# Kernel tuning notes

Measured on AMD Instinct MI355X. Metric: run time of the kernel, lower is better.

Reference implementation:

```python
import jax, jax.numpy as jnp
import numpy as np

NUM_HEAD = 8

def _ln(h, g, b):
    m = jnp.mean(h, axis=-1, keepdims=True)
    v = jnp.mean(jnp.square(h - m), axis=-1, keepdims=True)
    return (h - m) * jax.lax.rsqrt(v + 1e-5) * g + b

def _lin(h, W, b):
    return h @ W.T + b

def _styl(h, e, se_w, se_b, sn_g, sn_b, so_w, so_b):
    # StylizationBlock (AdaLN-zero): emb -> SiLU -> Linear -> scale/shift
    eo = _lin(jax.nn.silu(e), se_w, se_b)[:, None, :]  # [B,1,2D]
    scale, shift = jnp.split(eo, 2, axis=-1)
    h = _ln(h, sn_g, sn_b) * (1.0 + scale) + shift
    return _lin(jax.nn.silu(h), so_w, so_b)

def setup_inputs():
    key = jax.random.key(0)
    ks = iter(jax.random.split(key, 48))
    T, B, N, D = 256, 64, 77, 512
    FF_SA, FF = 1024, 2048
    w = lambda *s: jax.random.normal(next(ks), s, dtype=jnp.float32) * 0.02
    z = lambda *s: jnp.zeros(s, jnp.float32)
    o = lambda *s: jnp.ones(s, jnp.float32)
    return dict(
        x=jax.random.normal(next(ks), (T, B, D), dtype=jnp.float32),
        xf=jax.random.normal(next(ks), (N, B, D), dtype=jnp.float32),
        emb=jax.random.normal(next(ks), (1, B, D), dtype=jnp.float32),
        sa_in_w=w(3 * D, D), sa_in_b=z(3 * D), sa_out_w=w(D, D), sa_out_b=z(D),
        sa_l1_w=w(FF_SA, D), sa_l1_b=z(FF_SA), sa_l2_w=w(D, FF_SA), sa_l2_b=z(D),
        sa_n1_g=o(D), sa_n1_b=z(D), sa_n2_g=o(D), sa_n2_b=z(D),
        ca_norm_g=o(D), ca_norm_b=z(D), ca_tnorm_g=o(D), ca_tnorm_b=z(D),
        ca_q_w=w(D, D), ca_q_b=z(D), ca_k_w=w(D, D), ca_k_b=z(D), ca_v_w=w(D, D), ca_v_b=z(D),
        ca_se_w=w(2 * D, D), ca_se_b=z(2 * D), ca_sn_g=o(D), ca_sn_b=z(D), ca_so_w=w(D, D), ca_so_b=z(D),
        ff_l1_w=w(FF, D), ff_l1_b=z(FF), ff_l2_w=w(D, FF), ff_l2_b=z(D),
        ff_se_w=w(2 * D, D), ff_se_b=z(2 * D), ff_sn_g=o(D), ff_sn_b=z(D), ff_so_w=w(D, D), ff_so_b=z(D),
    )

def reference(x, xf, emb, sa_in_w, sa_in_b, sa_out_w, sa_out_b, sa_l1_w, sa_l1_b, sa_l2_w, sa_l2_b, sa_n1_g, sa_n1_b, sa_n2_g, sa_n2_b, ca_norm_g, ca_norm_b, ca_tnorm_g, ca_tnorm_b, ca_q_w, ca_q_b, ca_k_w, ca_k_b, ca_v_w, ca_v_b, ca_se_w, ca_se_b, ca_sn_g, ca_sn_b, ca_so_w, ca_so_b, ff_l1_w, ff_l1_b, ff_l2_w, ff_l2_b, ff_se_w, ff_se_b, ff_sn_g, ff_sn_b, ff_so_w, ff_so_b):
    T = x.shape[0]
    # --- MLD self-attention path: concat motion tokens, text tokens, time emb ---
    src = jnp.concatenate([x, xf, emb], axis=0)  # [S,B,D], S = T+N+1
    S, B, D = src.shape
    dh = D // NUM_HEAD
    qkv = _lin(src, sa_in_w, sa_in_b)
    q, k, v = jnp.split(qkv, 3, axis=-1)
    q = q.reshape(S, B, NUM_HEAD, dh) * (dh ** -0.5)
    k = k.reshape(S, B, NUM_HEAD, dh)
    v = v.reshape(S, B, NUM_HEAD, dh)
    att = jax.nn.softmax(jnp.einsum('sbhd,tbhd->bhst', q, k), axis=-1)
    o = jnp.einsum('bhst,tbhd->sbhd', att, v).reshape(S, B, D)
    src = _ln(src + _lin(o, sa_out_w, sa_out_b), sa_n1_g, sa_n1_b)
    ffh = _lin(jax.nn.relu(_lin(src, sa_l1_w, sa_l1_b)), sa_l2_w, sa_l2_b)
    src = _ln(src + ffh, sa_n2_g, sa_n2_b)
    xb = src[:T].transpose(1, 0, 2)   # [B,T,D]
    xfb = xf.transpose(1, 0, 2)       # [B,N,D]
    eb = emb[0]                       # [B,D]
    # --- Linear temporal cross-attention ---
    xn = _ln(xb, ca_norm_g, ca_norm_b)
    tn = _ln(xfb, ca_tnorm_g, ca_tnorm_b)
    qc = jax.nn.softmax(_lin(xn, ca_q_w, ca_q_b).reshape(B, T, NUM_HEAD, dh), axis=-1)
    kc = jax.nn.softmax(_lin(tn, ca_k_w, ca_k_b).reshape(B, -1, NUM_HEAD, dh), axis=1)
    vc = _lin(tn, ca_v_w, ca_v_b).reshape(B, -1, NUM_HEAD, dh)
    ctx = jnp.einsum('bnhd,bnhl->bhdl', kc, vc)
    y = jnp.einsum('bthd,bhdl->bthl', qc, ctx).reshape(B, T, D)
    xb = xb + _styl(y, eb, ca_se_w, ca_se_b, ca_sn_g, ca_sn_b, ca_so_w, ca_so_b)
    # --- FFN with stylization ---
    y = _lin(jax.nn.gelu(_lin(xb, ff_l1_w, ff_l1_b), approximate=False), ff_l2_w, ff_l2_b)
    xb = xb + _styl(y, eb, ff_se_w, ff_se_b, ff_sn_g, ff_sn_b, ff_so_w, ff_so_b)
    return xb.transpose(1, 0, 2)  # [T,B,D]
```

## Files before the change

### kernel.cpp

```cpp
#include <hip/hip_runtime.h>
#include <hip/hip_bf16.h>
#include <cstddef>

#define TT 256
#define BB 64
#define NN 77
#define DD 512
#define SS 334
#define HH 8
#define M1 (SS*BB)
#define M2 (BB*TT)
#define FF 2048

#define REG 10944512ULL

typedef __attribute__((ext_vector_type(4))) float f32x4;
typedef __attribute__((ext_vector_type(8))) short bf16x8;
typedef __attribute__((ext_vector_type(8))) unsigned short u16x8;

__device__ inline unsigned short f2bf(float f) {
  __hip_bfloat16 h = __float2bfloat16(f);
  return *reinterpret_cast<unsigned short*>(&h);
}
__device__ inline float bf2f(unsigned short u) {
  return __uint_as_float(((unsigned)u) << 16);
}

__global__ __launch_bounds__(256) void cvt4_kernel(
    const float* s0, unsigned short* d0, int n0,
    const float* s1, unsigned short* d1, int n1,
    const float* s2, unsigned short* d2, int n2,
    const float* s3, unsigned short* d3, int n3) {
  const float* s; unsigned short* d; int n;
  switch (blockIdx.y) {
    case 0: s = s0; d = d0; n = n0; break;
    case 1: s = s1; d = d1; n = n1; break;
    case 2: s = s2; d = d2; n = n2; break;
    default: s = s3; d = d3; n = n3; break;
  }
  for (int i = (blockIdx.x * 256 + threadIdx.x) * 4; i < n; i += gridDim.x * 1024) {
    float4 v = *(const float4*)(s + i);
    ushort4 u;
    u.x = f2bf(v.x); u.y = f2bf(v.y); u.z = f2bf(v.z); u.w = f2bf(v.w);
    *(ushort4*)(d + i) = u;
  }
}

__global__ __launch_bounds__(256) void concat_src_kernel(
    const float* __restrict__ x, const float* __restrict__ xf,
    const float* __restrict__ emb, float* __restrict__ src,
    unsigned short* __restrict__ srcbf) {
  int idx = blockIdx.x * 256 + threadIdx.x;
  if (idx >= SS * BB * 128) return;
  int c4 = idx & 127;
  int row = idx >> 7;
  int s = row >> 6, b = row & 63;
  const float* p;
  if (s < TT)            p = x   + ((size_t)(s * BB + b)) * DD;
  else if (s < TT + NN)  p = xf  + ((size_t)((s - TT) * BB + b)) * DD;
  else                   p = emb + (size_t)b * DD;
  float4 v = ((const float4*)p)[c4];
  ((float4*)(src + (size_t)row * DD))[c4] = v;
  ushort4 u;
  u.x = f2bf(v.x); u.y = f2bf(v.y); u.z = f2bf(v.z); u.w = f2bf(v.w);
  ((ushort4*)(srcbf + (size_t)row * DD))[c4] = u;
}

template<int EPI, bool CBF>
__global__ __launch_bounds__(256) void gemm_bf(
    const unsigned short* __restrict__ A, const unsigned short* __restrict__ W,
    const float* __restrict__ bias, void* __restrict__ Cp_, void* __restrict__ C2,
    int M, int K, int ldc) {
  __shared__ unsigned short As[8][128][8];
  __shared__ unsigned short Bs[8][128][8];
  const int tid = threadIdx.x;
  int bxt, byt;
  {
    int total = gridDim.x * gridDim.y;
    int raw = blockIdx.y * gridDim.x + blockIdx.x;
    if ((total & 7) == 0) {
      int lid = (raw & 7) * (total >> 3) + (raw >> 3);
      bxt = lid % gridDim.x;
      byt = lid / gridDim.x;
    } else { bxt = blockIdx.x; byt = blockIdx.y; }
  }
  const int bm = byt * 128;
  const int bn = bxt * 128;
  const int lane = tid & 63;
  const int wave = tid >> 6;
  const int wr = wave >> 1, wc = wave & 1;
  const int q = lane >> 4, lr = lane & 15;

  f32x4 acc[4][4];
#pragma unroll
  for (int m = 0; m < 4; ++m)
#pragma unroll
    for (int n = 0; n < 4; ++n) acc[m][n] = (f32x4){0.f, 0.f, 0.f, 0.f};

  const int srow = tid >> 1;
  const int sk = (tid & 1) * 32;
  const int c0 = (tid & 1) * 4;
  int arow = bm + srow; if (arow >= M) arow = M - 1;
  const unsigned short* Ag = A + (size_t)arow * K + sk;
  const unsigned short* Wg = W + (size_t)(bn + srow) * K + sk;

  for (int k0 = 0; k0 < K; k0 += 64) {
    u16x8 a0 = *(const u16x8*)(Ag + k0);
    u16x8 a1 = *(const u16x8*)(Ag + k0 + 8);
    u16x8 a2 = *(const u16x8*)(Ag + k0 + 16);
    u16x8 a3 = *(const u16x8*)(Ag + k0 + 24);
    u16x8 b0 = *(const u16x8*)(Wg + k0);
    u16x8 b1 = *(const u16x8*)(Wg + k0 + 8);
    u16x8 b2 = *(const u16x8*)(Wg + k0 + 16);
    u16x8 b3 = *(const u16x8*)(Wg + k0 + 24);
    __syncthreads();
    *(u16x8*)&As[c0 + 0][srow][0] = a0;
    *(u16x8*)&As[c0 + 1][srow][0] = a1;
    *(u16x8*)&As[c0 + 2][srow][0] = a2;
    *(u16x8*)&As[c0 + 3][srow][0] = a3;
    *(u16x8*)&Bs[c0 + 0][srow][0] = b0;
    *(u16x8*)&Bs[c0 + 1][srow][0] = b1;
    *(u16x8*)&Bs[c0 + 2][srow][0] = b2;
    *(u16x8*)&Bs[c0 + 3][srow][0] = b3;
    __syncthreads();
#pragma unroll
    for (int ks = 0; ks < 2; ++ks) {
      bf16x8 af[4], bf[4];
#pragma unroll
      for (int m = 0; m < 4; ++m)
        af[m] = *(const bf16x8*)&As[ks * 4 + q][wr * 64 + m * 16 + lr][0];
#pragma unroll
      for (int n = 0; n < 4; ++n)
        bf[n] = *(const bf16x8*)&Bs[ks * 4 + q][wc * 64 + n * 16 + lr][0];
#pragma unroll
      for (int m = 0; m < 4; ++m)
#pragma unroll
        for (int n = 0; n < 4; ++n)
          acc[m][n] = __builtin_amdgcn_mfma_f32_16x16x32_bf16(af[m], bf[n], acc[m][n], 0, 0, 0);
    }
  }

  if (EPI == 6) {
    const int hcol = (bn >> 6) + wc;
#pragma unroll
    for (int m = 0; m < 4; ++m) {
#pragma unroll
      for (int i = 0; i < 4; ++i) {
        float vv[4];
        float mx = -1e30f;
#pragma unroll
        for (int n = 0; n < 4; ++n) {
          float v = acc[m][n][i] + bias[bn + wc * 64 + n * 16 + lr];
          vv[n] = v; mx = fmaxf(mx, v);
        }
#pragma unroll
        for (int off = 8; off; off >>= 1) mx = fmaxf(mx, __shfl_xor(mx, off));
        float sum = 0.f;
#pragma unroll
        for (int n = 0; n < 4; ++n) { vv[n] = __expf(vv[n] - mx); sum += vv[n]; }
#pragma unroll
        for (int off = 8; off; off >>= 1) sum += __shfl_xor(sum, off);
        float inv = 1.f / sum;
        const int row = bm + wr * 64 + m * 16 + q * 4 + i;
        const int t = row & 255, b2 = row >> 8;
        unsigned short* dst =
            (unsigned short*)Cp_ + (((size_t)(b2 * 8 + hcol) * 256 + t) << 6);
#pragma unroll
        for (int n = 0; n < 4; ++n)
          dst[n * 16 + lr] = f2bf(vv[n] * inv);
      }
    }
    return;
  }

#pragma unroll
  for (int m = 0; m < 4; ++m) {
#pragma unroll
    for (int n = 0; n < 4; ++n) {
      const int col = bn + wc * 64 + n * 16 + lr;
      const float bb = bias[col];
#pragma unroll
      for (int i = 0; i < 4; ++i) {
        const int row = bm + wr * 64 + m * 16 + q * 4 + i;
        if (row < M) {
          float v = acc[m][n][i] + bb;
          if (EPI == 1) v = fmaxf(v, 0.f);
          if (EPI == 2) v = 0.5f * v * (1.f + erff(v * 0.70710678118f));
          if (EPI == 7) v *= 0.125f;
          if (EPI <= 2 || EPI == 7) {
            if (CBF) ((unsigned short*)Cp_)[(size_t)row * ldc + col] = f2bf(v);
            else     ((float*)Cp_)[(size_t)row * ldc + col] = v;
          } else if (EPI == 3) {
            ((float*)Cp_)[(size_t)row * ldc + col] += v;
          } else if (EPI == 4) {
            float* C = (float*)Cp_ + (size_t)row * ldc + col;
            float o = *C + v; *C = o;
            ((unsigned short*)C2)[(size_t)row * ldc + col] = f2bf(o);
          } else {
            float o = ((const float*)Cp_)[(size_t)row * ldc + col] + v;
            int t = row & 255, b2 = row >> 8;
            ((float*)C2)[((size_t)(t * BB + b2)) * DD + col] = o;
          }
        }
      }
    }
  }
}

__global__ __launch_bounds__(256) void attn_mfma_kernel(
    const unsigned short* __restrict__ Qb, const unsigned short* __restrict__ KVb,
    unsigned short* __restrict__ Ob) {
  __shared__ unsigned short Qs[256][72];
  __shared__ unsigned short Ks[64][72];
  __shared__ unsigned short Vt[64][72];
  __shared__ unsigned short Ps[4][16][72];
  const int bh = blockIdx.x, b = bh >> 3, h = bh & 7;
  const int tid = threadIdx.x;
  const int wave = tid >> 6, lane = tid & 63;
  const int q = lane >> 4, lr = lane & 15;
  const int sr = tid >> 2;
  const int c0 = (tid & 3) << 4;
#pragma unroll
  for (int it = 0; it < 8; ++it) {
    int v = it * 256 + tid;
    int row = v >> 3, col = (v & 7) * 8;
    u16x8 d8 = *(const u16x8*)(Qb + ((size_t)(row * BB + b)) * 512 + h * 64 + col);
    *(u16x8*)&Qs[row][col] = d8;
  }
  f32x4 oacc[4][4];
#pragma unroll
  for (int m = 0; m < 4; ++m)
#pragma unroll
    for (int dt = 0; dt < 4; ++dt) oacc[m][dt] = (f32x4){0.f, 0.f, 0.f, 0.f};
  float m_r[4][4], l_r[4][4];
#pragma unroll
  for (int m = 0; m < 4; ++m)
#pragma unroll
    for (int i = 0; i < 4; ++i) { m_r[m][i] = -1e30f; l_r[m][i] = 0.f; }

  for (int kt = 0; kt < 6; ++kt) {
    __syncthreads();
    {
      int t = kt * 64 + sr;
      u16x8 k0 = {0, 0, 0, 0, 0, 0, 0, 0}, k1 = k0, w0 = k0, w1 = k0;
      if (t < SS) {
        const unsigned short* kp = KVb + ((size_t)(t * BB + b)) * 1024 + h * 64 + c0;
        k0 = *(const u16x8*)kp; k1 = *(const u16x8*)(kp + 8);
        w0 = *(const u16x8*)(kp + 512); w1 = *(const u16x8*)(kp + 520);
      }
      *(u16x8*)&Ks[sr][c0] = k0;
      *(u16x8*)&Ks[sr][c0 + 8] = k1;
#pragma unroll
      for (int j = 0; j < 8; ++j) Vt[c0 + j][sr] = w0[j];
#pragma unroll
      for (int j = 0; j < 8; ++j) Vt[c0 + 8 + j][sr] = w1[j];
    }
    __syncthreads();
#pragma unroll
    for (int m = 0; m < 4; ++m) {
      f32x4 sacc[4];
#pragma unroll
      for (int ct = 0; ct < 4; ++ct) sacc[ct] = (f32x4){0.f, 0.f, 0.f, 0.f};
#pragma unroll
      for (int kc = 0; kc < 2; ++kc) {
        bf16x8 aq = *(const bf16x8*)&Qs[wave * 64 + m * 16 + lr][kc * 32 + q * 8];
#pragma unroll
        for (int ct = 0; ct < 4; ++ct) {
          bf16x8 bk = *(const bf16x8*)&Ks[ct * 16 + lr][kc * 32 + q * 8];
          sacc[ct] = __builtin_amdgcn_mfma_f32_16x16x32_bf16(aq, bk, sacc[ct], 0, 0, 0);
        }
      }
      if (kt == 5) {
#pragma unroll
        for (int ct = 0; ct < 4; ++ct)
          if (320 + ct * 16 + lr >= SS) {
#pragma unroll
            for (int i = 0; i < 4; ++i) sacc[ct][i] = -1e30f;
          }
      }
      float pexp[4][4];
#pragma unroll
      for (int i = 0; i < 4; ++i) {
        float mt = fmaxf(fmaxf(sacc[0][i], sacc[1][i]), fmaxf(sacc[2][i], sacc[3][i]));
#pragma unroll
        for (int off = 8; off; off >>= 1) mt = fmaxf(mt, __shfl_xor(mt, off));
        float mn = fmaxf(m_r[m][i], mt);
        float rescale = __expf(m_r[m][i] - mn);
        m_r[m][i] = mn;
        float se = 0.f;
#pragma unroll
        for (int ct = 0; ct < 4; ++ct) {
          float e = __expf(sacc[ct][i] - mn);
          pexp[ct][i] = e;
          se += e;
        }
#pragma unroll
        for (int off = 8; off; off >>= 1) se += __shfl_xor(se, off);
        l_r[m][i] = l_r[m][i] * rescale + se;
#pragma unroll
        for (int dt = 0; dt < 4; ++dt) oacc[m][dt][i] *= rescale;
      }
#pragma unroll
      for (int ct = 0; ct < 4; ++ct)
#pragma unroll
        for (int i = 0; i < 4; ++i)
          Ps[wave][q * 4 + i][ct * 16 + lr] = f2bf(pexp[ct][i]);
#pragma unroll
      for (int kc = 0; kc < 2; ++kc) {
        bf16x8 ap = *(const bf16x8*)&Ps[wave][lr][kc * 32 + q * 8];
#pragma unroll
        for (int dt = 0; dt < 4; ++dt) {
          bf16x8 bv = *(const bf16x8*)&Vt[dt * 16 + lr][kc * 32 + q * 8];
          oacc[m][dt] = __builtin_amdgcn_mfma_f32_16x16x32_bf16(ap, bv, oacc[m][dt], 0, 0, 0);
        }
      }
    }
  }
#pragma unroll
  for (int m = 0; m < 4; ++m) {
#pragma unroll
    for (int i = 0; i < 4; ++i) {
      int s = wave * 64 + m * 16 + q * 4 + i;
      float inv = 1.f / l_r[m][i];
      unsigned short* op = Ob + ((size_t)(s * BB + b)) * 512 + h * 64;
#pragma unroll
      for (int dt = 0; dt < 4; ++dt)
        op[dt * 16 + lr] = f2bf(oacc[m][dt][i] * inv);
    }
  }
}

__global__ __launch_bounds__(256) void lin_y_mfma(
    const unsigned short* __restrict__ qch, const unsigned short* __restrict__ ctxT,
    float* __restrict__ y) {
  __shared__ unsigned short Qs[256][72];
  __shared__ unsigned short Cs[64][72];
  const int bh = blockIdx.x, b = bh >> 3, h = bh & 7;
  const int tid = threadIdx.x;
  const int wave = tid >> 6, lane = tid & 63;
  const int q = lane >> 4, lr = lane & 15;
  {
    const unsigned short* qp = qch + (size_t)bh * 16384;
#pragma unroll
    for (int it = 0; it < 8; ++it) {
      int v = it * 256 + tid;
      u16x8 d8 = *(const u16x8*)(qp + v * 8);
      *(u16x8*)&Qs[v >> 3][(v & 7) * 8] = d8;
    }
    const unsigned short* cp = ctxT + (size_t)bh * 4096;
#pragma unroll
    for (int it = 0; it < 2; ++it) {
      int v = it * 256 + tid;
      u16x8 d8 = *(const u16x8*)(cp + v * 8);
      *(u16x8*)&Cs[v >> 3][(v & 7) * 8] = d8;
    }
  }
  __syncthreads();
  f32x4 acc[4][4];
#pragma unroll
  for (int m = 0; m < 4; ++m)
#pragma unroll
    for (int n = 0; n < 4; ++n) acc[m][n] = (f32x4){0.f, 0.f, 0.f, 0.f};
#pragma unroll
  for (int kc = 0; kc < 2; ++kc) {
    bf16x8 af[4], bf[4];
#pragma unroll
    for (int m = 0; m < 4; ++m)
      af[m] = *(const bf16x8*)&Qs[wave * 64 + m * 16 + lr][kc * 32 + q * 8];
#pragma unroll
    for (int n = 0; n < 4; ++n)
      bf[n] = *(const bf16x8*)&Cs[n * 16 + lr][kc * 32 + q * 8];
#pragma unroll
    for (int m = 0; m < 4; ++m)
#pragma unroll
      for (int n = 0; n < 4; ++n)
        acc[m][n] = __builtin_amdgcn_mfma_f32_16x16x32_bf16(af[m], bf[n], acc[m][n], 0, 0, 0);
  }
#pragma unroll
  for (int m = 0; m < 4; ++m) {
#pragma unroll
    for (int n = 0; n < 4; ++n) {
#pragma unroll
      for (int i = 0; i < 4; ++i) {
        int t = wave * 64 + m * 16 + q * 4 + i;
        y[((size_t)(b * TT + t)) * DD + h * 64 + n * 16 + lr] = acc[m][n][i];
      }
    }
  }
}

__global__ __launch_bounds__(256) void gemm_se_kernel(
    const float* __restrict__ emb,
    const float* __restrict__ w0, const float* __restrict__ b0, float* __restrict__ c0_,
    const float* __restrict__ w1, const float* __restrict__ b1, float* __restrict__ c1_) {
  __shared__ float As[16][64];
  __shared__ float Ws[16][64];
  const float* W    = blockIdx.y ? w1 : w0;
  const float* bias = blockIdx.y ? b1 : b0;
  float* C          = blockIdx.y ? c1_ : c0_;
  const int tid = threadIdx.x;
  const int bn = blockIdx.x << 6;
  const int lr = tid >> 2;
  const int lk = (tid & 3) << 2;
  const float* Ap = emb + (size_t)lr * 512 + lk;
  const float* Wp = W + (size_t)(bn + lr) * 512 + lk;
  const int tx = tid & 15, ty = tid >> 4;
  float c[4][4] = {};
  for (int k0 = 0; k0 < 512; k0 += 16) {
    float4 av = *(const float4*)(Ap + k0);
    av.x = av.x / (1.f + __expf(-av.x));
    av.y = av.y / (1.f + __expf(-av.y));
    av.z = av.z / (1.f + __expf(-av.z));
    av.w = av.w / (1.f + __expf(-av.w));
    float4 wv = *(const float4*)(Wp + k0);
    __syncthreads();
    As[lk + 0][lr] = av.x; As[lk + 1][lr] = av.y;
    As[lk + 2][lr] = av.z; As[lk + 3][lr] = av.w;
    Ws[lk + 0][lr] = wv.x; Ws[lk + 1][lr] = wv.y;
    Ws[lk + 2][lr] = wv.z; Ws[lk + 3][lr] = wv.w;
    __syncthreads();
#pragma unroll
    for (int k = 0; k < 16; ++k) {
      const float4 a = *(const float4*)&As[k][ty << 2];
      const float4 w = *(const float4*)&Ws[k][tx << 2];
      c[0][0] += a.x * w.x; c[0][1] += a.x * w.y; c[0][2] += a.x * w.z; c[0][3] += a.x * w.w;
      c[1][0] += a.y * w.x; c[1][1] += a.y * w.y; c[1][2] += a.y * w.z; c[1][3] += a.y * w.w;
      c[2][0] += a.z * w.x; c[2][1] += a.z * w.y; c[2][2] += a.z * w.z; c[2][3] += a.z * w.w;
      c[3][0] += a.w * w.x; c[3][1] += a.w * w.y; c[3][2] += a.w * w.z; c[3][3] += a.w * w.w;
    }
  }
#pragma unroll
  for (int i = 0; i < 4; ++i) {
    int row = (ty << 2) + i;
    float* Cp = C + (size_t)row * 1024 + bn + (tx << 2);
#pragma unroll
    for (int j = 0; j < 4; ++j)
      Cp[j] = c[i][j] + bias[bn + (tx << 2) + j];
  }
}

__global__ __launch_bounds__(64) void ln_kernel(
    const float* __restrict__ in, const float* __restrict__ res,
    float* __restrict__ out, const float* __restrict__ g,
    const float* __restrict__ beta, unsigned short* __restrict__ obf) {
  const int row = blockIdx.x;
  const int lane = threadIdx.x;
  const float* ip = in + (size_t)row * DD;
  float v[8];
  float s = 0.f, ss = 0.f;
#pragma unroll
  for (int u = 0; u < 2; ++u) {
    int d = u * 256 + lane * 4;
    float4 a = *(const float4*)(ip + d);
    if (res) {
      float4 r = *(const float4*)(res + (size_t)row * DD + d);
      a.x += r.x; a.y += r.y; a.z += r.z; a.w += r.w;
    }
    v[u * 4 + 0] = a.x; v[u * 4 + 1] = a.y; v[u * 4 + 2] = a.z; v[u * 4 + 3] = a.w;
    s += a.x + a.y + a.z + a.w;
    ss += a.x * a.x + a.y * a.y + a.z * a.z + a.w * a.w;
  }
#pragma unroll
  for (int off = 32; off; off >>= 1) { s += __shfl_xor(s, off); ss += __shfl_xor(ss, off); }
  float mean = s * (1.f / 512.f);
  float var = ss * (1.f / 512.f) - mean * mean;
  float rstd = rsqrtf(var + 1e-5f);
  float* op = out + (size_t)row * DD;
#pragma unroll
  for (int u = 0; u < 2; ++u) {
    int d = u * 256 + lane * 4;
    float4 o4;
    o4.x = (v[u * 4 + 0] - mean) * rstd * g[d + 0] + beta[d + 0];
    o4.y = (v[u * 4 + 1] - mean) * rstd * g[d + 1] + beta[d + 1];
    o4.z = (v[u * 4 + 2] - mean) * rstd * g[d + 2] + beta[d + 2];
    o4.w = (v[u * 4 + 3] - mean) * rstd * g[d + 3] + beta[d + 3];
    *(float4*)(op + d) = o4;
    if (obf) {
      ushort4 u4;
      u4.x = f2bf(o4.x); u4.y = f2bf(o4.y); u4.z = f2bf(o4.z); u4.w = f2bf(o4.w);
      *(ushort4*)(obf + (size_t)row * DD + d) = u4;
    }
  }
}

template<bool WF32>
__global__ __launch_bounds__(64) void t2bln_kernel(
    const float* __restrict__ in, float* __restrict__ raw,
    unsigned short* __restrict__ obf, const float* __restrict__ g,
    const float* __restrict__ beta, int Rr) {
  const int rp = blockIdx.x;
  const int b = rp / Rr, r = rp % Rr;
  const float* ip = in + ((size_t)(r * BB + b)) * DD;
  const int lane = threadIdx.x;
  float v[8];
  float s = 0.f, ss = 0.f;
#pragma unroll
  for (int u = 0; u < 2; ++u) {
    int d = u * 256 + lane * 4;
    float4 a = *(const float4*)(ip + d);
    if (WF32) *(float4*)(raw + (size_t)rp * DD + d) = a;
    v[u * 4 + 0] = a.x; v[u * 4 + 1] = a.y; v[u * 4 + 2] = a.z; v[u * 4 + 3] = a.w;
    s += a.x + a.y + a.z + a.w;
    ss += a.x * a.x + a.y * a.y + a.z * a.z + a.w * a.w;
  }
#pragma unroll
  for (int off = 32; off; off >>= 1) { s += __shfl_xor(s, off); ss += __shfl_xor(ss, off); }
  float mean = s * (1.f / 512.f);
  float var = ss * (1.f / 512.f) - mean * mean;
  float rstd = rsqrtf(var + 1e-5f);
#pragma unroll
  for (int u = 0; u < 2; ++u) {
    int d = u * 256 + lane * 4;
    ushort4 u4;
    u4.x = f2bf((v[u * 4 + 0] - mean) * rstd * g[d + 0] + beta[d + 0]);
    u4.y = f2bf((v[u * 4 + 1] - mean) * rstd * g[d + 1] + beta[d + 1]);
    u4.z = f2bf((v[u * 4 + 2] - mean) * rstd * g[d + 2] + beta[d + 2]);
    u4.w = f2bf((v[u * 4 + 3] - mean) * rstd * g[d + 3] + beta[d + 3]);
    *(ushort4*)(obf + (size_t)rp * DD + d) = u4;
  }
}

__global__ __launch_bounds__(64) void styl_kernel(
    const float* __restrict__ y, const float* __restrict__ eo,
    const float* __restrict__ g, const float* __restrict__ beta,
    unsigned short* __restrict__ out) {
  const int row = blockIdx.x;
  const int b = row >> 8;
  const int lane = threadIdx.x;
  const float* ip = y + (size_t)row * DD;
  const float* sc = eo + (size_t)b * 1024;
  float v[8];
  float s = 0.f, ss = 0.f;
#pragma unroll
  for (int u = 0; u < 2; ++u) {
    int d = u * 256 + lane * 4;
    float4 a = *(const float4*)(ip + d);
    v[u * 4 + 0] = a.x; v[u * 4 + 1] = a.y; v[u * 4 + 2] = a.z; v[u * 4 + 3] = a.w;
    s += a.x + a.y + a.z + a.w;
    ss += a.x * a.x + a.y * a.y + a.z * a.z + a.w * a.w;
  }
#pragma unroll
  for (int off = 32; off; off >>= 1) { s += __shfl_xor(s, off); ss += __shfl_xor(ss, off); }
  float mean = s * (1.f / 512.f);
  float var = ss * (1.f / 512.f) - mean * mean;
  float rstd = rsqrtf(var + 1e-5f);
#pragma unroll
  for (int u = 0; u < 2; ++u) {
    int d0 = u * 256 + lane * 4;
    ushort4 u4;
#pragma unroll
    for (int j = 0; j < 4; ++j) {
      int d = d0 + j;
      float ln = (v[u * 4 + j] - mean) * rstd * g[d] + beta[d];
      float h = ln * (1.f + sc[d]) + sc[512 + d];
      float r = h / (1.f + __expf(-h));
      ((unsigned short*)&u4)[j] = f2bf(r);
    }
    *(ushort4*)(out + (size_t)row * DD + d0) = u4;
  }
}

__global__ __launch_bounds__(256) void softmax_n_kernel(float* __restrict__ a) {
  int b = blockIdx.x;
  int c = blockIdx.y * 256 + threadIdx.x;
  float* p = a + ((size_t)b * NN) * DD + c;
  float m = -1e30f;
  for (int n = 0; n < NN; ++n) m = fmaxf(m, p[(size_t)n * DD]);
  float sum = 0.f;
  for (int n = 0; n < NN; ++n) sum += __expf(p[(size_t)n * DD] - m);
  float inv = 1.f / sum;
  for (int n = 0; n < NN; ++n) p[(size_t)n * DD] = __expf(p[(size_t)n * DD] - m) * inv;
}

__global__ __launch_bounds__(256) void ctx_kernel(
    const float* __restrict__ kc, const float* __restrict__ vc,
    unsigned short* __restrict__ ctxT) {
  __shared__ float ks[NN][64];
  __shared__ float vs[NN][64];
  int bh = blockIdx.x; int b = bh >> 3, h = bh & 7;
  for (int l = threadIdx.x; l < NN * 64; l += 256) {
    int n = l >> 6, d = l & 63;
    size_t idx = ((size_t)(b * NN + n)) * DD + h * 64 + d;
    ks[n][d] = kc[idx];
    vs[n][d] = vc[idx];
  }
  __syncthreads();
  int d = threadIdx.x >> 2;
  int l0 = (threadIdx.x & 3) << 4;
  float acc[16] = {};
  for (int n = 0; n < NN; ++n) {
    float kd = ks[n][d];
#pragma unroll
    for (int j = 0; j < 16; ++j) acc[j] += kd * vs[n][l0 + j];
  }
  unsigned short* cp = ctxT + (size_t)bh * 4096 + d;
#pragma unroll
  for (int j = 0; j < 16; ++j) cp[(size_t)(l0 + j) * 64] = f2bf(acc[j]);
}

extern "C" void kernel_launch(void* const* d_in, const int* in_sizes, int n_in,
                              void* d_out, int out_size, void* d_ws, size_t ws_size,
                              hipStream_t stream) {
  const float* x       = (const float*)d_in[0];
  const float* xf      = (const float*)d_in[1];
  const float* emb     = (const float*)d_in[2];
  const float* sa_in_w = (const float*)d_in[3];
  const float* sa_in_b = (const float*)d_in[4];
  const float* sa_out_w= (const float*)d_in[5];
  const float* sa_out_b= (const float*)d_in[6];
  const float* sa_l1_w = (const float*)d_in[7];
  const float* sa_l1_b = (const float*)d_in[8];
  const float* sa_l2_w = (const float*)d_in[9];
  const float* sa_l2_b = (const float*)d_in[10];
  const float* sa_n1_g = (const float*)d_in[11];
  const float* sa_n1_b = (const float*)d_in[12];
  const float* sa_n2_g = (const float*)d_in[13];
  const float* sa_n2_b = (const float*)d_in[14];
  const float* ca_norm_g = (const float*)d_in[15];
  const float* ca_norm_b = (const float*)d_in[16];
  const float* ca_tnorm_g= (const float*)d_in[17];
  const float* ca_tnorm_b= (const float*)d_in[18];
  const float* ca_q_w  = (const float*)d_in[19];
  const float* ca_q_b  = (const float*)d_in[20];
  const float* ca_k_w  = (const float*)d_in[21];
  const float* ca_k_b  = (const float*)d_in[22];
  const float* ca_v_w  = (const float*)d_in[23];
  const float* ca_v_b  = (const float*)d_in[24];
  const float* ca_se_w = (const float*)d_in[25];
  const float* ca_se_b = (const float*)d_in[26];
  const float* ca_sn_g = (const float*)d_in[27];
  const float* ca_sn_b = (const float*)d_in[28];
  const float* ca_so_w = (const float*)d_in[29];
  const float* ca_so_b = (const float*)d_in[30];
  const float* ff_l1_w = (const float*)d_in[31];
  const float* ff_l1_b = (const float*)d_in[32];
  const float* ff_l2_w = (const float*)d_in[33];
  const float* ff_l2_b = (const float*)d_in[34];
  const float* ff_se_w = (const float*)d_in[35];
  const float* ff_se_b = (const float*)d_in[36];
  const float* ff_sn_g = (const float*)d_in[37];
  const float* ff_sn_b = (const float*)d_in[38];
  const float* ff_so_w = (const float*)d_in[39];
  const float* ff_so_b = (const float*)d_in[40];

  float* R1 = (float*)d_ws;
  float* R2 = R1 + REG;
  float* R3 = R2 + REG;
  float* dof = (float*)d_out;

  unsigned short* w_sa_in  = (unsigned short*)dof;
  unsigned short* w_sa_out = w_sa_in + 786432;
  unsigned short* w_sa_l1  = w_sa_out + 262144;
  unsigned short* w_sa_l2  = w_sa_l1 + 524288;
  unsigned short* srcbf    = (unsigned short*)(dof + 1048576);
  unsigned short* w_ca_q  = (unsigned short*)(R2 + 8552448);
  unsigned short* w_ca_k  = w_ca_q + 262144;
  unsigned short* w_ca_v  = w_ca_k + 262144;
  unsigned short* w_ca_so = w_ca_v + 262144;
  unsigned short* w_ff_l1 = (unsigned short*)(R2 + 9076736);
  unsigned short* w_ff_l2 = w_ff_l1 + 1048576;
  unsigned short* w_ff_so = w_ff_l2 + 1048576;

  float* src = R1;
  unsigned short* Qbf  = (unsigned short*)R3;
  unsigned short* Obf  = (unsigned short*)(R3 + 5472256);
  unsigned short* KVbf = (unsigned short*)R2;
  float* proj  = R2;
  unsigned short* h1bf = (unsigned short*)R2;
  float* proj2 = R3;
  float* xb = R3;
  unsigned short* xnbf = (unsigned short*)R2;
  unsigned short* tnbf = (unsigned short*)(R2 + 4194304);
  unsigned short* qch = (unsigned short*)dof;
  float* kc  = R1;
  float* vc  = R1 + 2523136;
  unsigned short* ctxTbf = (unsigned short*)(R1 + 5046272);
  float* eo  = R2 + 8421376;
  float* eo2 = eo + 65536;
  float* yb  = R2;
  unsigned short* hstbf = (unsigned short*)R1;
  unsigned short* xbbf  = (unsigned short*)(R1 + 4194304);
  unsigned short* g1bf = (unsigned short*)R2;
  float* y2 = R1;
  unsigned short* hst2bf = (unsigned short*)R2;

  cvt4_kernel<<<dim3(1024, 4), 256, 0, stream>>>(
      sa_in_w, w_sa_in, 786432, sa_out_w, w_sa_out, 262144,
      sa_l1_w, w_sa_l1, 524288, sa_l2_w, w_sa_l2, 524288);
  concat_src_kernel<<<10688, 256, 0, stream>>>(x, xf, emb, src, srcbf);
  gemm_bf<7, true><<<dim3(4, 128), 256, 0, stream>>>(
      srcbf, w_sa_in, sa_in_b, Qbf, nullptr, M2, 512, 512);
  gemm_bf<0, true><<<dim3(8, 167), 256, 0, stream>>>(
      srcbf, w_sa_in + (size_t)512 * 512, sa_in_b + 512, KVbf, nullptr, M1, 512, 1024);
  attn_mfma_kernel<<<BB * HH, 256, 0, stream>>>(Qbf, KVbf, Obf);
  gemm_bf<0, false><<<dim3(4, 128), 256, 0, stream>>>(
      Obf, w_sa_out, sa_out_b, proj, nullptr, M2, 512, 512);
  ln_kernel<<<M2, 64, 0, stream>>>(src, proj, src, sa_n1_g, sa_n1_b, srcbf);
  gemm_bf<1, true><<<dim3(8, 128), 256, 0, stream>>>(
      srcbf, w_sa_l1, sa_l1_b, h1bf, nullptr, M2, 512, 1024);
  gemm_bf<0, false><<<dim3(4, 128), 256, 0, stream>>>(
      h1bf, w_sa_l2, sa_l2_b, proj2, nullptr, M2, 1024, 512);
  cvt4_kernel<<<dim3(1024, 4), 256, 0, stream>>>(
      ca_q_w, w_ca_q, 262144, ca_k_w, w_ca_k, 262144,
      ca_v_w, w_ca_v, 262144, ca_so_w, w_ca_so, 262144);
  cvt4_kernel<<<dim3(1024, 4), 256, 0, stream>>>(
      ff_l1_w, w_ff_l1, 1048576, ff_l2_w, w_ff_l2, 1048576,
      ff_so_w, w_ff_so, 262144, nullptr, nullptr, 0);
  ln_kernel<<<M2, 64, 0, stream>>>(src, proj2, src, sa_n2_g, sa_n2_b, nullptr);

  t2bln_kernel<true><<<M2, 64, 0, stream>>>(src, xb, xnbf, ca_norm_g, ca_norm_b, TT);
  gemm_bf<6, false><<<dim3(4, 128), 256, 0, stream>>>(
      xnbf, w_ca_q, ca_q_b, qch, nullptr, M2, 512, 512);
  t2bln_kernel<false><<<BB * NN, 64, 0, stream>>>(xf, nullptr, tnbf, ca_tnorm_g, ca_tnorm_b, NN);
  gemm_bf<0, false><<<dim3(4, 39), 256, 0, stream>>>(
      tnbf, w_ca_k, ca_k_b, kc, nullptr, BB * NN, 512, 512);
  softmax_n_kernel<<<dim3(64, 2), 256, 0, stream>>>(kc);
  gemm_bf<0, false><<<dim3(4, 39), 256, 0, stream>>>(
      tnbf, w_ca_v, ca_v_b, vc, nullptr, BB * NN, 512, 512);
  ctx_kernel<<<BB * HH, 256, 0, stream>>>(kc, vc, ctxTbf);
  gemm_se_kernel<<<dim3(16, 2), 256, 0, stream>>>(
      emb, ca_se_w, ca_se_b, eo, ff_se_w, ff_se_b, eo2);
  lin_y_mfma<<<BB * HH, 256, 0, stream>>>(qch, ctxTbf, yb);
  styl_kernel<<<M2, 64, 0, stream>>>(yb, eo, ca_sn_g, ca_sn_b, hstbf);
  gemm_bf<4, false><<<dim3(4, 128), 256, 0, stream>>>(
      hstbf, w_ca_so, ca_so_b, xb, xbbf, M2, 512, 512);

  for (int hlf = 0; hlf < 2; ++hlf) {
    size_t m0 = (size_t)hlf * 8192;
    gemm_bf<2, true><<<dim3(16, 64), 256, 0, stream>>>(
        xbbf + m0 * DD, w_ff_l1, ff_l1_b, g1bf, nullptr, 8192, 512, 2048);
    gemm_bf<0, false><<<dim3(4, 64), 256, 0, stream>>>(
        g1bf, w_ff_l2, ff_l2_b, y2 + m0 * DD, nullptr, 8192, 2048, 512);
  }
  styl_kernel<<<M2, 64, 0, stream>>>(y2, eo2, ff_sn_g, ff_sn_b, hst2bf);
  gemm_bf<5, false><<<dim3(4, 128), 256, 0, stream>>>(
      hst2bf, w_ff_so, ff_so_b, xb, dof, M2, 512, 512);
}
```

Before: 678.5 us.

## Fuse residual LN with transpose LN, split attention over query halves, split FFN by hidden dim

Merges the second self-attention LayerNorm with the batch-major transpose and cross-attention LayerNorm into one kernel. This removes the fp32 copy of the residual stream, which now stays in [T,B,D] layout, with the GEMM epilogues indexing it directly. The attention kernel is split into two 128-query blocks per (batch, head) to double the grid and raise occupancy, at the cost of loading K/V twice. The FFN is restructured from two M-halves into two hidden-dim halves, using a new ldw stride and an accumulate epilogue (EPI 8), so the whole M dimension fits in each launch. The second half adds a read-modify-write on the fp32 output.

```diff
diff --git a/kernel.cpp b/kernel.cpp
--- a/kernel.cpp
+++ b/kernel.cpp
@@ -70,7 +70,7 @@
 __global__ __launch_bounds__(256) void gemm_bf(
     const unsigned short* __restrict__ A, const unsigned short* __restrict__ W,
     const float* __restrict__ bias, void* __restrict__ Cp_, void* __restrict__ C2,
-    int M, int K, int ldc) {
+    int M, int K, int ldw, int ldc) {
   __shared__ unsigned short As[8][128][8];
   __shared__ unsigned short Bs[8][128][8];
   const int tid = threadIdx.x;
@@ -102,7 +102,7 @@
   const int c0 = (tid & 1) * 4;
   int arow = bm + srow; if (arow >= M) arow = M - 1;
   const unsigned short* Ag = A + (size_t)arow * K + sk;
-  const unsigned short* Wg = W + (size_t)(bn + srow) * K + sk;
+  const unsigned short* Wg = W + (size_t)(bn + srow) * ldw + sk;
 
   for (int k0 = 0; k0 < K; k0 += 64) {
     u16x8 a0 = *(const u16x8*)(Ag + k0);
@@ -178,7 +178,7 @@
 #pragma unroll
     for (int n = 0; n < 4; ++n) {
       const int col = bn + wc * 64 + n * 16 + lr;
-      const float bb = bias[col];
+      const float bb = (EPI == 8) ? 0.f : bias[col];
 #pragma unroll
       for (int i = 0; i < 4; ++i) {
         const int row = bm + wr * 64 + m * 16 + q * 4 + i;
@@ -190,16 +190,18 @@
           if (EPI <= 2 || EPI == 7) {
             if (CBF) ((unsigned short*)Cp_)[(size_t)row * ldc + col] = f2bf(v);
             else     ((float*)Cp_)[(size_t)row * ldc + col] = v;
-          } else if (EPI == 3) {
+          } else if (EPI == 3 || EPI == 8) {
             ((float*)Cp_)[(size_t)row * ldc + col] += v;
           } else if (EPI == 4) {
-            float* C = (float*)Cp_ + (size_t)row * ldc + col;
+            const int t = row & 255, b2 = row >> 8;
+            float* C = (float*)Cp_ + ((size_t)(t * BB + b2)) * DD + col;
             float o = *C + v; *C = o;
             ((unsigned short*)C2)[(size_t)row * ldc + col] = f2bf(o);
           } else {
-            float o = ((const float*)Cp_)[(size_t)row * ldc + col] + v;
-            int t = row & 255, b2 = row >> 8;
-            ((float*)C2)[((size_t)(t * BB + b2)) * DD + col] = o;
+            const int t = row & 255, b2 = row >> 8;
+            const size_t idx = ((size_t)(t * BB + b2)) * DD + col;
+            float o = ((const float*)Cp_)[idx] + v;
+            ((float*)C2)[idx] = o;
           }
         }
       }
@@ -210,31 +212,32 @@
 __global__ __launch_bounds__(256) void attn_mfma_kernel(
     const unsigned short* __restrict__ Qb, const unsigned short* __restrict__ KVb,
     unsigned short* __restrict__ Ob) {
-  __shared__ unsigned short Qs[256][72];
+  __shared__ unsigned short Qs[128][72];
   __shared__ unsigned short Ks[64][72];
   __shared__ unsigned short Vt[64][72];
   __shared__ unsigned short Ps[4][16][72];
-  const int bh = blockIdx.x, b = bh >> 3, h = bh & 7;
+  const int bh = blockIdx.y, b = bh >> 3, h = bh & 7;
+  const int s0 = blockIdx.x << 7;
   const int tid = threadIdx.x;
   const int wave = tid >> 6, lane = tid & 63;
   const int q = lane >> 4, lr = lane & 15;
   const int sr = tid >> 2;
   const int c0 = (tid & 3) << 4;
 #pragma unroll
-  for (int it = 0; it < 8; ++it) {
+  for (int it = 0; it < 4; ++it) {
     int v = it * 256 + tid;
     int row = v >> 3, col = (v & 7) * 8;
-    u16x8 d8 = *(const u16x8*)(Qb + ((size_t)(row * BB + b)) * 512 + h * 64 + col);
+    u16x8 d8 = *(const u16x8*)(Qb + ((size_t)((s0 + row) * BB + b)) * 512 + h * 64 + col);
     *(u16x8*)&Qs[row][col] = d8;
   }
-  f32x4 oacc[4][4];
-#pragma unroll
-  for (int m = 0; m < 4; ++m)
+  f32x4 oacc[2][4];
+#pragma unroll
+  for (int m = 0; m < 2; ++m)
 #pragma unroll
     for (int dt = 0; dt < 4; ++dt) oacc[m][dt] = (f32x4){0.f, 0.f, 0.f, 0.f};
-  float m_r[4][4], l_r[4][4];
-#pragma unroll
-  for (int m = 0; m < 4; ++m)
+  float m_r[2][4], l_r[2][4];
+#pragma unroll
+  for (int m = 0; m < 2; ++m)
 #pragma unroll
     for (int i = 0; i < 4; ++i) { m_r[m][i] = -1e30f; l_r[m][i] = 0.f; }
 
@@ -257,13 +260,13 @@
     }
     __syncthreads();
 #pragma unroll
-    for (int m = 0; m < 4; ++m) {
+    for (int m = 0; m < 2; ++m) {
       f32x4 sacc[4];
 #pragma unroll
       for (int ct = 0; ct < 4; ++ct) sacc[ct] = (f32x4){0.f, 0.f, 0.f, 0.f};
 #pragma unroll
       for (int kc = 0; kc < 2; ++kc) {
-        bf16x8 aq = *(const bf16x8*)&Qs[wave * 64 + m * 16 + lr][kc * 32 + q * 8];
+        bf16x8 aq = *(const bf16x8*)&Qs[wave * 32 + m * 16 + lr][kc * 32 + q * 8];
 #pragma unroll
         for (int ct = 0; ct < 4; ++ct) {
           bf16x8 bk = *(const bf16x8*)&Ks[ct * 16 + lr][kc * 32 + q * 8];
@@ -317,10 +320,10 @@
     }
   }
 #pragma unroll
-  for (int m = 0; m < 4; ++m) {
+  for (int m = 0; m < 2; ++m) {
 #pragma unroll
     for (int i = 0; i < 4; ++i) {
-      int s = wave * 64 + m * 16 + q * 4 + i;
+      int s = s0 + wave * 32 + m * 16 + q * 4 + i;
       float inv = 1.f / l_r[m][i];
       unsigned short* op = Ob + ((size_t)(s * BB + b)) * 512 + h * 64;
 #pragma unroll
@@ -483,11 +486,67 @@
   }
 }
 
-template<bool WF32>
+__global__ __launch_bounds__(64) void t2bln_res_kernel(
+    float* __restrict__ src, const float* __restrict__ proj2,
+    unsigned short* __restrict__ xnbf,
+    const float* __restrict__ g2, const float* __restrict__ b2,
+    const float* __restrict__ gca, const float* __restrict__ bca) {
+  const int row = blockIdx.x;
+  const int t = row >> 6, b = row & 63;
+  const size_t soff = (size_t)row * DD;
+  const int lane = threadIdx.x;
+  float v[8];
+  float s = 0.f, ss = 0.f;
+#pragma unroll
+  for (int u = 0; u < 2; ++u) {
+    int d = u * 256 + lane * 4;
+    float4 a = *(const float4*)(src + soff + d);
+    float4 r = *(const float4*)(proj2 + soff + d);
+    a.x += r.x; a.y += r.y; a.z += r.z; a.w += r.w;
+    v[u * 4 + 0] = a.x; v[u * 4 + 1] = a.y; v[u * 4 + 2] = a.z; v[u * 4 + 3] = a.w;
+    s += a.x + a.y + a.z + a.w;
+    ss += a.x * a.x + a.y * a.y + a.z * a.z + a.w * a.w;
+  }
+#pragma unroll
+  for (int off = 32; off; off >>= 1) { s += __shfl_xor(s, off); ss += __shfl_xor(ss, off); }
+  float mean = s * (1.f / 512.f);
+  float var = ss * (1.f / 512.f) - mean * mean;
+  float rstd = rsqrtf(var + 1e-5f);
+  float s2 = 0.f, ss2 = 0.f;
+#pragma unroll
+  for (int u = 0; u < 8; ++u) {
+    int d = (u >> 2) * 256 + lane * 4 + (u & 3);
+    float o = (v[u] - mean) * rstd * g2[d] + b2[d];
+    v[u] = o;
+    s2 += o; ss2 += o * o;
+  }
+#pragma unroll
+  for (int u = 0; u < 2; ++u) {
+    int d = u * 256 + lane * 4;
+    float4 o4 = {v[u * 4 + 0], v[u * 4 + 1], v[u * 4 + 2], v[u * 4 + 3]};
+    *(float4*)(src + soff + d) = o4;
+  }
+#pragma unroll
+  for (int off = 32; off; off >>= 1) { s2 += __shfl_xor(s2, off); ss2 += __shfl_xor(ss2, off); }
+  float mean2 = s2 * (1.f / 512.f);
+  float var2 = ss2 * (1.f / 512.f) - mean2 * mean2;
+  float rstd2 = rsqrtf(var2 + 1e-5f);
+  const size_t orow = (size_t)(b * TT + t) * DD;
+#pragma unroll
+  for (int u = 0; u < 2; ++u) {
+    int d = u * 256 + lane * 4;
+    ushort4 u4;
+    u4.x = f2bf((v[u * 4 + 0] - mean2) * rstd2 * gca[d + 0] + bca[d + 0]);
+    u4.y = f2bf((v[u * 4 + 1] - mean2) * rstd2 * gca[d + 1] + bca[d + 1]);
+    u4.z = f2bf((v[u * 4 + 2] - mean2) * rstd2 * gca[d + 2] + bca[d + 2]);
+    u4.w = f2bf((v[u * 4 + 3] - mean2) * rstd2 * gca[d + 3] + bca[d + 3]);
+    *(ushort4*)(xnbf + orow + d) = u4;
+  }
+}
+
 __global__ __launch_bounds__(64) void t2bln_kernel(
-    const float* __restrict__ in, float* __restrict__ raw,
-    unsigned short* __restrict__ obf, const float* __restrict__ g,
-    const float* __restrict__ beta, int Rr) {
+    const float* __restrict__ in, unsigned short* __restrict__ obf,
+    const float* __restrict__ g, const float* __restrict__ beta, int Rr) {
   const int rp = blockIdx.x;
   const int b = rp / Rr, r = rp % Rr;
   const float* ip = in + ((size_t)(r * BB + b)) * DD;
@@ -498,7 +557,6 @@
   for (int u = 0; u < 2; ++u) {
     int d = u * 256 + lane * 4;
     float4 a = *(const float4*)(ip + d);
-    if (WF32) *(float4*)(raw + (size_t)rp * DD + d) = a;
     v[u * 4 + 0] = a.x; v[u * 4 + 1] = a.y; v[u * 4 + 2] = a.z; v[u * 4 + 3] = a.w;
     s += a.x + a.y + a.z + a.w;
     ss += a.x * a.x + a.y * a.y + a.z * a.z + a.w * a.w;
@@ -668,71 +726,72 @@
   float* proj  = R2;
   unsigned short* h1bf = (unsigned short*)R2;
   float* proj2 = R3;
-  float* xb = R3;
+  float* xbt = R1;
   unsigned short* xnbf = (unsigned short*)R2;
   unsigned short* tnbf = (unsigned short*)(R2 + 4194304);
   unsigned short* qch = (unsigned short*)dof;
-  float* kc  = R1;
-  float* vc  = R1 + 2523136;
-  unsigned short* ctxTbf = (unsigned short*)(R1 + 5046272);
+  float* kc  = R3;
+  float* vc  = R3 + 2523136;
+  unsigned short* ctxTbf = (unsigned short*)(R3 + 5046272);
+  unsigned short* hstbf = (unsigned short*)(R3 + 6094848);
+  unsigned short* xbbf  = (unsigned short*)(R3 + 8192000);
   float* eo  = R2 + 8421376;
   float* eo2 = eo + 65536;
   float* yb  = R2;
-  unsigned short* hstbf = (unsigned short*)R1;
-  unsigned short* xbbf  = (unsigned short*)(R1 + 4194304);
   unsigned short* g1bf = (unsigned short*)R2;
-  float* y2 = R1;
-  unsigned short* hst2bf = (unsigned short*)R2;
+  float* y2 = dof;
+  unsigned short* hst2bf = (unsigned short*)R3;
 
   cvt4_kernel<<<dim3(1024, 4), 256, 0, stream>>>(
       sa_in_w, w_sa_in, 786432, sa_out_w, w_sa_out, 262144,
       sa_l1_w, w_sa_l1, 524288, sa_l2_w, w_sa_l2, 524288);
   concat_src_kernel<<<10688, 256, 0, stream>>>(x, xf, emb, src, srcbf);
   gemm_bf<7, true><<<dim3(4, 128), 256, 0, stream>>>(
-      srcbf, w_sa_in, sa_in_b, Qbf, nullptr, M2, 512, 512);
+      srcbf, w_sa_in, sa_in_b, Qbf, nullptr, M2, 512, 512, 512);
   gemm_bf<0, true><<<dim3(8, 167), 256, 0, stream>>>(
-      srcbf, w_sa_in + (size_t)512 * 512, sa_in_b + 512, KVbf, nullptr, M1, 512, 1024);
-  attn_mfma_kernel<<<BB * HH, 256, 0, stream>>>(Qbf, KVbf, Obf);
+      srcbf, w_sa_in + (size_t)512 * 512, sa_in_b + 512, KVbf, nullptr, M1, 512, 512, 1024);
+  attn_mfma_kernel<<<dim3(2, BB * HH), 256, 0, stream>>>(Qbf, KVbf, Obf);
   gemm_bf<0, false><<<dim3(4, 128), 256, 0, stream>>>(
-      Obf, w_sa_out, sa_out_b, proj, nullptr, M2, 512, 512);
+      Obf, w_sa_out, sa_out_b, proj, nullptr, M2, 512, 512, 512);
   ln_kernel<<<M2, 64, 0, stream>>>(src, proj, src, sa_n1_g, sa_n1_b, srcbf);
   gemm_bf<1, true><<<dim3(8, 128), 256, 0, stream>>>(
-      srcbf, w_sa_l1, sa_l1_b, h1bf, nullptr, M2, 512, 1024);
+      srcbf, w_sa_l1, sa_l1_b, h1bf, nullptr, M2, 512, 512, 1024);
   gemm_bf<0, false><<<dim3(4, 128), 256, 0, stream>>>(
-      h1bf, w_sa_l2, sa_l2_b, proj2, nullptr, M2, 1024, 512);
+      h1bf, w_sa_l2, sa_l2_b, proj2, nullptr, M2, 1024, 1024, 512);
   cvt4_kernel<<<dim3(1024, 4), 256, 0, stream>>>(
       ca_q_w, w_ca_q, 262144, ca_k_w, w_ca_k, 262144,
       ca_v_w, w_ca_v, 262144, ca_so_w, w_ca_so, 262144);
   cvt4_kernel<<<dim3(1024, 4), 256, 0, stream>>>(
       ff_l1_w, w_ff_l1, 1048576, ff_l2_w, w_ff_l2, 1048576,
       ff_so_w, w_ff_so, 262144, nullptr, nullptr, 0);
-  ln_kernel<<<M2, 64, 0, stream>>>(src, proj2, src, sa_n2_g, sa_n2_b, nullptr);
-
-  t2bln_kernel<true><<<M2, 64, 0, stream>>>(src, xb, xnbf, ca_norm_g, ca_norm_b, TT);
+  t2bln_res_kernel<<<M2, 64, 0, stream>>>(
+      src, proj2, xnbf, sa_n2_g, sa_n2_b, ca_norm_g, ca_norm_b);
+
   gemm_bf<6, false><<<dim3(4, 128), 256, 0, stream>>>(
-      xnbf, w_ca_q, ca_q_b, qch, nullptr, M2, 512, 512);
-  t2bln_kernel<false><<<BB * NN, 64, 0, stream>>>(xf, nullptr, tnbf, ca_tnorm_g, ca_tnorm_b, NN);
+      xnbf, w_ca_q, ca_q_b, qch, nullptr, M2, 512, 512, 512);
+  t2bln_kernel<<<BB * NN, 64, 0, stream>>>(xf, tnbf, ca_tnorm_g, ca_tnorm_b, NN);
   gemm_bf<0, false><<<dim3(4, 39), 256, 0, stream>>>(
-      tnbf, w_ca_k, ca_k_b, kc, nullptr, BB * NN, 512, 512);
+      tnbf, w_ca_k, ca_k_b, kc, nullptr, BB * NN, 512, 512, 512);
   softmax_n_kernel<<<dim3(64, 2), 256, 0, stream>>>(kc);
   gemm_bf<0, false><<<dim3(4, 39), 256, 0, stream>>>(
-      tnbf, w_ca_v, ca_v_b, vc, nullptr, BB * NN, 512, 512);
+      tnbf, w_ca_v, ca_v_b, vc, nullptr, BB * NN, 512, 512, 512);
   ctx_kernel<<<BB * HH, 256, 0, stream>>>(kc, vc, ctxTbf);
   gemm_se_kernel<<<dim3(16, 2), 256, 0, stream>>>(
       emb, ca_se_w, ca_se_b, eo, ff_se_w, ff_se_b, eo2);
   lin_y_mfma<<<BB * HH, 256, 0, stream>>>(qch, ctxTbf, yb);
   styl_kernel<<<M2, 64, 0, stream>>>(yb, eo, ca_sn_g, ca_sn_b, hstbf);
   gemm_bf<4, false><<<dim3(4, 128), 256, 0, stream>>>(
-      hstbf, w_ca_so, ca_so_b, xb, xbbf, M2, 512, 512);
-
-  for (int hlf = 0; hlf < 2; ++hlf) {
-    size_t m0 = (size_t)hlf * 8192;
-    gemm_bf<2, true><<<dim3(16, 64), 256, 0, stream>>>(
-        xbbf + m0 * DD, w_ff_l1, ff_l1_b, g1bf, nullptr, 8192, 512, 2048);
-    gemm_bf<0, false><<<dim3(4, 64), 256, 0, stream>>>(
-        g1bf, w_ff_l2, ff_l2_b, y2 + m0 * DD, nullptr, 8192, 2048, 512);
-  }
+      hstbf, w_ca_so, ca_so_b, xbt, xbbf, M2, 512, 512, 512);
+
+  gemm_bf<2, true><<<dim3(8, 128), 256, 0, stream>>>(
+      xbbf, w_ff_l1, ff_l1_b, g1bf, nullptr, M2, 512, 512, 1024);
+  gemm_bf<0, false><<<dim3(4, 128), 256, 0, stream>>>(
+      g1bf, w_ff_l2, ff_l2_b, y2, nullptr, M2, 1024, 2048, 512);
+  gemm_bf<2, true><<<dim3(8, 128), 256, 0, stream>>>(
+      xbbf, w_ff_l1 + (size_t)1024 * 512, ff_l1_b + 1024, g1bf, nullptr, M2, 512, 512, 1024);
+  gemm_bf<8, false><<<dim3(4, 128), 256, 0, stream>>>(
+      g1bf, w_ff_l2 + 1024, ff_l2_b, y2, nullptr, M2, 1024, 2048, 512);
   styl_kernel<<<M2, 64, 0, stream>>>(y2, eo2, ff_sn_g, ff_sn_b, hst2bf);
   gemm_bf<5, false><<<dim3(4, 128), 256, 0, stream>>>(
-      hst2bf, w_ff_so, ff_so_b, xb, dof, M2, 512, 512);
-}
+      hst2bf, w_ff_so, ff_so_b, xbt, dof, M2, 512, 512, 512);
+}
```

After: 646.4 us. -4.7%, faster.
